# Optimization experiments

Measured on AMD Instinct MI355X. Metric: run time of the kernel, lower is better.

## Reference

```python
import jax, jax.numpy as jnp
import numpy as np
from jax import lax

QMIN, QMAX = -127, 127  # symmetric int8 range matching lut randint(-127,128)


def setup_inputs() -> dict:
    key = jax.random.key(0)
    k1, k2, k3, k4 = jax.random.split(key, 4)
    x = jax.random.normal(k1, (8, 3, 128, 128), jnp.float32)
    weight = jax.random.normal(k2, (16, 3, 3, 3), jnp.float32) * 0.1
    bias = jax.random.normal(k3, (16,), jnp.float32) * 0.01
    scale_x = jnp.float32(0.05)   # trainable per-tensor activation scale
    scale_w = jnp.float32(0.005)  # trainable per-tensor weight scale
    # LUT: row (a+128)*256 + (b+128) holds the approximate product of int8 a,b
    # as two int8 bytes (hi, lo); torch stores int8, we keep values in int32.
    lut = jax.random.randint(k4, (256 * 256, 2), -127, 128, jnp.int32)
    return {"x": x, "weight": weight, "bias": bias,
            "scale_x": scale_x, "scale_w": scale_w, "lut": lut}


def _lut_products(lut):
    # combine (hi, lo) int8 bytes into a 16-bit product value, [65536]
    hi = lut[:, 0].astype(jnp.int32)
    lo = lut[:, 1].astype(jnp.int32) & 255  # low byte is unsigned
    return hi * 256 + lo


def _approx_conv_int(qx, qw, lut):
    # qx: [B,Cin,H,W] int32 in [-127,127]; qw: [O,Cin,K,K] int32
    O = qw.shape[0]
    F = qw.shape[1] * qw.shape[2] * qw.shape[3]
    # im2col: [B, Cin*K*K, H, W], feature dim ordered (Cin, kh, kw)
    patches = lax.conv_general_dilated_patches(
        qx.astype(jnp.float32), (3, 3), (1, 1), ((1, 1), (1, 1))
    ).astype(jnp.int32)
    ip = patches + 128                      # [B, F, H, W], in [1,255]
    iw = qw.reshape(O, F) + 128             # [O, F]
    idx = ip[:, None] * 256 + iw[None, :, :, None, None]  # [B,O,F,H,W]
    prod = _lut_products(lut)[idx]          # gathered approx products, int32
    return prod.sum(axis=2)                 # [B, O, H, W] int32 accumulator


def reference(x, weight, bias, scale_x, scale_w, lut):
    # per-tensor int8 quantization
    qx = jnp.clip(jnp.round(x / scale_x), QMIN, QMAX).astype(jnp.int32)
    qw = jnp.clip(jnp.round(weight / scale_w), QMIN, QMAX).astype(jnp.int32)
    acc = _approx_conv_int(qx, qw, lut)     # LUT-approximated int conv
    out = acc.astype(jnp.float32) * (scale_x * scale_w)
    return out + bias[None, :, None, None]
```

## Files before the change

### kernel.cpp

```cpp
#include <hip/hip_runtime.h>

#define B_    8
#define CIN   3
#define OC    16
#define HH    128
#define WW    128
#define KK    3
#define FF    27
#define NSITE (B_*HH*WW)
#define OGRP  4
#define NGRP  (OC/OGRP)
#define MBLK  512
#define PH    130
#define PLANE (PH*PH)
#define QA_BYTES (B_*CIN*PLANE)
#define T4_BYTES (NGRP*FF*256*4*2)
#define SLAB_INT4 (FF*256*4*2/16)

__global__ void prep_kernel(const float* __restrict__ x,
                            const float* __restrict__ wgt,
                            const float* __restrict__ sx_p,
                            const float* __restrict__ sw_p,
                            const int*   __restrict__ lut,
                            short*       __restrict__ T4,
                            unsigned char* __restrict__ qa)
{
    const int i = blockIdx.x * blockDim.x + threadIdx.x;

    if (i < B_ * CIN * PLANE) {
        int bc = i / PLANE;
        int p  = i - bc * PLANE;
        int hp = p / PH;
        int wp = p - hp * PH;
        int h  = hp - 1;
        int w  = wp - 1;
        unsigned char v = 128;
        if ((unsigned)h < HH && (unsigned)w < WW) {
            float q = rintf(x[(bc * HH + h) * WW + w] / sx_p[0]);
            q = fminf(127.f, fmaxf(-127.f, q));
            v = (unsigned char)((int)q + 128);
        }
        qa[i] = v;
    }

    if (i < NGRP * FF * 256) {
        int og = i / (FF * 256);
        int r  = i - og * (FF * 256);
        int f  = r >> 8;
        int a  = r & 255;
        int vals[4];
        #pragma unroll
        for (int ol = 0; ol < 4; ++ol) {
            int o = og * OGRP + ol;
            float q = rintf(wgt[o * FF + f] / sw_p[0]);
            q = fminf(127.f, fmaxf(-127.f, q));
            int iw  = (int)q + 128;
            int row = (a << 8) | iw;
            int hi  = lut[2 * row];
            int lo  = lut[2 * row + 1] & 255;
            vals[ol] = hi * 256 + lo;
        }
        int2 d;
        d.x = (vals[1] << 16) | (vals[0] & 0xffff);
        d.y = (vals[3] << 16) | (vals[2] & 0xffff);
        *reinterpret_cast<int2*>(T4 + (size_t)i * 4) = d;
    }
}

__global__ __launch_bounds__(MBLK, 4) void conv_kernel(
    const unsigned char* __restrict__ qa,
    const short* __restrict__ T4,
    const float* __restrict__ bias,
    const float* __restrict__ sx_p,
    const float* __restrict__ sw_p,
    float*       __restrict__ out)
{
    __shared__ int2 colv[FF * 256];

    const int og   = blockIdx.x & 3;
    const int sblk = blockIdx.x >> 2;

    {
        const int4* __restrict__ src =
            reinterpret_cast<const int4*>(T4 + (size_t)og * FF * 256 * 4);
        int4* dst = reinterpret_cast<int4*>(colv);
        for (int c = threadIdx.x; c < SLAB_INT4; c += MBLK)
            dst[c] = src[c];
    }
    __syncthreads();

    const int s  = sblk * MBLK + threadIdx.x;
    const int b  = s >> 14;
    const int hw = s & 16383;
    const int h  = hw >> 7;
    const int w  = hw & 127;

    int av[FF];
    #pragma unroll
    for (int c = 0; c < CIN; ++c) {
        const unsigned char* __restrict__ bp =
            qa + (b * CIN + c) * PLANE + h * PH + w;
        #pragma unroll
        for (int kh = 0; kh < KK; ++kh)
            #pragma unroll
            for (int kw = 0; kw < KK; ++kw)
                av[c * 9 + kh * 3 + kw] = bp[kh * PH + kw];
    }

    int acc0 = 0, acc1 = 0, acc2 = 0, acc3 = 0;
    #pragma unroll
    for (int f = 0; f < FF; ++f) {
        int2 d = colv[f * 256 + av[f]];
        acc0 += (short)d.x;
        acc1 += d.x >> 16;
        acc2 += (short)d.y;
        acc3 += d.y >> 16;
    }

    const float sxw = sx_p[0] * sw_p[0];
    const int   ob  = og * OGRP;
    float* op = out + ((b * OC + ob) * HH + h) * WW + w;
    op[0 * HH * WW] = (float)acc0 * sxw + bias[ob + 0];
    op[1 * HH * WW] = (float)acc1 * sxw + bias[ob + 1];
    op[2 * HH * WW] = (float)acc2 * sxw + bias[ob + 2];
    op[3 * HH * WW] = (float)acc3 * sxw + bias[ob + 3];
}

extern "C" void kernel_launch(void* const* d_in, const int* in_sizes, int n_in,
                              void* d_out, int out_size, void* d_ws, size_t ws_size,
                              hipStream_t stream)
{
    const float* x    = (const float*)d_in[0];
    const float* wgt  = (const float*)d_in[1];
    const float* bias = (const float*)d_in[2];
    const float* sx   = (const float*)d_in[3];
    const float* sw   = (const float*)d_in[4];
    const int*   lut  = (const int*)d_in[5];

    char* ws = (char*)d_ws;
    short*         T4 = (short*)ws;
    unsigned char* qa = (unsigned char*)(ws + T4_BYTES);

    prep_kernel<<<(B_ * CIN * PLANE + 255) / 256, 256, 0, stream>>>(
        x, wgt, sx, sw, lut, T4, qa);

    conv_kernel<<<(NSITE / MBLK) * NGRP, MBLK, 0, stream>>>(
        qa, T4, bias, sx, sw, (float*)d_out);
}
```

Before: 76.24 us.

## Fuse prep and conv into one cooperative persistent kernel with grid sync

Merges the quantization/LUT-table prep kernel and the conv kernel into a single cooperative launch. Prep work is spread grid-stride across a persistent grid, and a grid-wide barrier separates it from the conv phase. Each block now handles two 512-site passes per shared-memory LUT slab load. The intent is to remove the second launch and its gap, and to amortise the slab copy over more sites. The cost is grid-sync overhead, a persistent grid sized from the occupancy query, and cooperative-launch constraints.

```diff
diff --git a/kernel.cpp b/kernel.cpp
--- a/kernel.cpp
+++ b/kernel.cpp
@@ -1,4 +1,7 @@
 #include <hip/hip_runtime.h>
+#include <hip/hip_cooperative_groups.h>
+
+namespace cg = cooperative_groups;
 
 #define B_    8
 #define CIN   3
@@ -13,117 +16,130 @@
 #define MBLK  512
 #define PH    130
 #define PLANE (PH*PH)
-#define QA_BYTES (B_*CIN*PLANE)
+#define QA_ELEMS (B_*CIN*PLANE)
 #define T4_BYTES (NGRP*FF*256*4*2)
+#define T4_ENT   (NGRP*FF*256)
 #define SLAB_INT4 (FF*256*4*2/16)
+#define NJOB  ((NSITE/(2*MBLK))*NGRP)
 
-__global__ void prep_kernel(const float* __restrict__ x,
-                            const float* __restrict__ wgt,
-                            const float* __restrict__ sx_p,
-                            const float* __restrict__ sw_p,
-                            const int*   __restrict__ lut,
-                            short*       __restrict__ T4,
-                            unsigned char* __restrict__ qa)
-{
-    const int i = blockIdx.x * blockDim.x + threadIdx.x;
-
-    if (i < B_ * CIN * PLANE) {
-        int bc = i / PLANE;
-        int p  = i - bc * PLANE;
-        int hp = p / PH;
-        int wp = p - hp * PH;
-        int h  = hp - 1;
-        int w  = wp - 1;
-        unsigned char v = 128;
-        if ((unsigned)h < HH && (unsigned)w < WW) {
-            float q = rintf(x[(bc * HH + h) * WW + w] / sx_p[0]);
-            q = fminf(127.f, fmaxf(-127.f, q));
-            v = (unsigned char)((int)q + 128);
-        }
-        qa[i] = v;
-    }
-
-    if (i < NGRP * FF * 256) {
-        int og = i / (FF * 256);
-        int r  = i - og * (FF * 256);
-        int f  = r >> 8;
-        int a  = r & 255;
-        int vals[4];
-        #pragma unroll
-        for (int ol = 0; ol < 4; ++ol) {
-            int o = og * OGRP + ol;
-            float q = rintf(wgt[o * FF + f] / sw_p[0]);
-            q = fminf(127.f, fmaxf(-127.f, q));
-            int iw  = (int)q + 128;
-            int row = (a << 8) | iw;
-            int hi  = lut[2 * row];
-            int lo  = lut[2 * row + 1] & 255;
-            vals[ol] = hi * 256 + lo;
-        }
-        int2 d;
-        d.x = (vals[1] << 16) | (vals[0] & 0xffff);
-        d.y = (vals[3] << 16) | (vals[2] & 0xffff);
-        *reinterpret_cast<int2*>(T4 + (size_t)i * 4) = d;
-    }
-}
-
-__global__ __launch_bounds__(MBLK, 4) void conv_kernel(
-    const unsigned char* __restrict__ qa,
-    const short* __restrict__ T4,
+__global__ __launch_bounds__(MBLK, 4) void fused_kernel(
+    const float* __restrict__ x,
+    const float* __restrict__ wgt,
     const float* __restrict__ bias,
     const float* __restrict__ sx_p,
     const float* __restrict__ sw_p,
+    const int*   __restrict__ lut,
+    short*       __restrict__ T4,
+    unsigned char* __restrict__ qa,
     float*       __restrict__ out)
 {
     __shared__ int2 colv[FF * 256];
 
-    const int og   = blockIdx.x & 3;
-    const int sblk = blockIdx.x >> 2;
+    const int gtid    = blockIdx.x * MBLK + threadIdx.x;
+    const int gstride = gridDim.x * MBLK;
 
     {
-        const int4* __restrict__ src =
-            reinterpret_cast<const int4*>(T4 + (size_t)og * FF * 256 * 4);
-        int4* dst = reinterpret_cast<int4*>(colv);
-        for (int c = threadIdx.x; c < SLAB_INT4; c += MBLK)
-            dst[c] = src[c];
-    }
-    __syncthreads();
-
-    const int s  = sblk * MBLK + threadIdx.x;
-    const int b  = s >> 14;
-    const int hw = s & 16383;
-    const int h  = hw >> 7;
-    const int w  = hw & 127;
-
-    int av[FF];
-    #pragma unroll
-    for (int c = 0; c < CIN; ++c) {
-        const unsigned char* __restrict__ bp =
-            qa + (b * CIN + c) * PLANE + h * PH + w;
-        #pragma unroll
-        for (int kh = 0; kh < KK; ++kh)
-            #pragma unroll
-            for (int kw = 0; kw < KK; ++kw)
-                av[c * 9 + kh * 3 + kw] = bp[kh * PH + kw];
+        const float sx = sx_p[0];
+        for (int i = gtid; i < QA_ELEMS; i += gstride) {
+            int bc = i / PLANE;
+            int p  = i - bc * PLANE;
+            int hp = p / PH;
+            int wp = p - hp * PH;
+            int h  = hp - 1;
+            int w  = wp - 1;
+            unsigned char v = 128;
+            if ((unsigned)h < HH && (unsigned)w < WW) {
+                float q = rintf(x[(bc * HH + h) * WW + w] / sx);
+                q = fminf(127.f, fmaxf(-127.f, q));
+                v = (unsigned char)((int)q + 128);
+            }
+            qa[i] = v;
+        }
     }
 
-    int acc0 = 0, acc1 = 0, acc2 = 0, acc3 = 0;
-    #pragma unroll
-    for (int f = 0; f < FF; ++f) {
-        int2 d = colv[f * 256 + av[f]];
-        acc0 += (short)d.x;
-        acc1 += d.x >> 16;
-        acc2 += (short)d.y;
-        acc3 += d.y >> 16;
+    {
+        const float sw = sw_p[0];
+        for (int i = gtid; i < T4_ENT; i += gstride) {
+            int og = i / (FF * 256);
+            int r  = i - og * (FF * 256);
+            int f  = r >> 8;
+            int a  = r & 255;
+            int vals[4];
+            #pragma unroll
+            for (int ol = 0; ol < 4; ++ol) {
+                int o = og * OGRP + ol;
+                float q = rintf(wgt[o * FF + f] / sw);
+                q = fminf(127.f, fmaxf(-127.f, q));
+                int iw  = (int)q + 128;
+                int row = (a << 8) | iw;
+                int hi  = lut[2 * row];
+                int lo  = lut[2 * row + 1] & 255;
+                vals[ol] = hi * 256 + lo;
+            }
+            int2 d;
+            d.x = (vals[1] << 16) | (vals[0] & 0xffff);
+            d.y = (vals[3] << 16) | (vals[2] & 0xffff);
+            *reinterpret_cast<int2*>(T4 + (size_t)i * 4) = d;
+        }
     }
 
+    __threadfence();
+    cg::this_grid().sync();
+
     const float sxw = sx_p[0] * sw_p[0];
-    const int   ob  = og * OGRP;
-    float* op = out + ((b * OC + ob) * HH + h) * WW + w;
-    op[0 * HH * WW] = (float)acc0 * sxw + bias[ob + 0];
-    op[1 * HH * WW] = (float)acc1 * sxw + bias[ob + 1];
-    op[2 * HH * WW] = (float)acc2 * sxw + bias[ob + 2];
-    op[3 * HH * WW] = (float)acc3 * sxw + bias[ob + 3];
+
+    for (int job = blockIdx.x; job < NJOB; job += gridDim.x) {
+        const int og  = job & 3;
+        const int sb2 = job >> 2;
+
+        __syncthreads();
+        {
+            const int4* __restrict__ src =
+                reinterpret_cast<const int4*>(T4 + (size_t)og * FF * 256 * 4);
+            int4* dst = reinterpret_cast<int4*>(colv);
+            for (int c = threadIdx.x; c < SLAB_INT4; c += MBLK)
+                dst[c] = src[c];
+        }
+        __syncthreads();
+
+        #pragma unroll
+        for (int pass = 0; pass < 2; ++pass) {
+            const int s  = (sb2 * 2 + pass) * MBLK + threadIdx.x;
+            const int b  = s >> 14;
+            const int hw = s & 16383;
+            const int h  = hw >> 7;
+            const int w  = hw & 127;
+
+            int av[FF];
+            #pragma unroll
+            for (int c = 0; c < CIN; ++c) {
+                const unsigned char* __restrict__ bp =
+                    qa + (b * CIN + c) * PLANE + h * PH + w;
+                #pragma unroll
+                for (int kh = 0; kh < KK; ++kh)
+                    #pragma unroll
+                    for (int kw = 0; kw < KK; ++kw)
+                        av[c * 9 + kh * 3 + kw] = bp[kh * PH + kw];
+            }
+
+            int acc0 = 0, acc1 = 0, acc2 = 0, acc3 = 0;
+            #pragma unroll
+            for (int f = 0; f < FF; ++f) {
+                int2 d = colv[f * 256 + av[f]];
+                acc0 += (short)d.x;
+                acc1 += d.x >> 16;
+                acc2 += (short)d.y;
+                acc3 += d.y >> 16;
+            }
+
+            const int ob = og * OGRP;
+            float* op = out + ((b * OC + ob) * HH + h) * WW + w;
+            op[0 * HH * WW] = (float)acc0 * sxw + bias[ob + 0];
+            op[1 * HH * WW] = (float)acc1 * sxw + bias[ob + 1];
+            op[2 * HH * WW] = (float)acc2 * sxw + bias[ob + 2];
+            op[3 * HH * WW] = (float)acc3 * sxw + bias[ob + 3];
+        }
+    }
 }
 
 extern "C" void kernel_launch(void* const* d_in, const int* in_sizes, int n_in,
@@ -138,12 +154,22 @@
     const int*   lut  = (const int*)d_in[5];
 
     char* ws = (char*)d_ws;
-    short*         T4 = (short*)ws;
-    unsigned char* qa = (unsigned char*)(ws + T4_BYTES);
+    short*         T4  = (short*)ws;
+    unsigned char* qa  = (unsigned char*)(ws + T4_BYTES);
+    float*         o   = (float*)d_out;
 
-    prep_kernel<<<(B_ * CIN * PLANE + 255) / 256, 256, 0, stream>>>(
-        x, wgt, sx, sw, lut, T4, qa);
+    static int grid = 0;
+    if (grid == 0) {
+        int nb = 0;
+        if (hipOccupancyMaxActiveBlocksPerMultiprocessor(
+                &nb, (const void*)fused_kernel, MBLK, 0) != hipSuccess || nb < 1)
+            nb = 1;
+        grid = nb * 256;
+        if (grid > NJOB) grid = NJOB;
+    }
 
-    conv_kernel<<<(NSITE / MBLK) * NGRP, MBLK, 0, stream>>>(
-        qa, T4, bias, sx, sw, (float*)d_out);
+    void* args[] = {(void*)&x, (void*)&wgt, (void*)&bias, (void*)&sx,
+                    (void*)&sw, (void*)&lut, (void*)&T4, (void*)&qa, (void*)&o};
+    hipLaunchCooperativeKernel((const void*)fused_kernel, dim3(grid), dim3(MBLK),
+                               args, 0, stream);
 }
```

Result: slower. 190.1 us (+149.3%).
